# Kernel optimization log

Measured on AMD Instinct MI355X. Metric: run time of the kernel, lower is better.

The kernel has to match this reference:

```python
import jax, jax.numpy as jnp
import numpy as np

B, L, V, H = 2, 2048, 1024, 16
HD = V // H  # head size 64
EPS = 1e-3   # keras LayerNormalization default


def setup_inputs() -> dict:
    key = jax.random.key(0)
    ks = jax.random.split(key, 10)
    scale = 1.0 / np.sqrt(V)
    return {
        "query": jax.random.normal(ks[0], (B, L, V), jnp.float32),
        "key_t": jax.random.normal(ks[1], (B, L, V), jnp.float32),
        "value": jax.random.normal(ks[2], (B, L, V), jnp.float32),
        "Wq": jax.random.normal(ks[3], (H, V, HD), jnp.float32) * scale,
        "Wk": jax.random.normal(ks[4], (H, V, HD), jnp.float32) * scale,
        "Wv": jax.random.normal(ks[5], (H, V, HD), jnp.float32) * scale,
        "gamma": jnp.ones((V,), jnp.float32),
        "beta": jnp.zeros((V,), jnp.float32),
        "query_mask": jax.random.randint(ks[6], (B, L), 0, 2, jnp.int32),
        "value_mask": jax.random.randint(ks[7], (B, L), 0, 2, jnp.int32),
    }


def reference(query, key_t, value, Wq, Wk, Wv, gamma, beta, query_mask, value_mask):
    qm = query_mask.astype(jnp.float32)  # (B,L)
    vm = value_mask.astype(jnp.float32)  # (B,L)

    # per-head no-bias Dense projections, batched over heads
    Q = jnp.einsum('blv,hvd->bhld', query, Wq)
    K = jnp.einsum('blv,hvd->bhld', key_t, Wk)
    Vh = jnp.einsum('blv,hvd->bhld', value, Wv)

    scores = jnp.einsum('bhld,bhmd->bhlm', Q, K) / jnp.sqrt(jnp.float32(HD))
    attn = jax.nn.softmax(scores, axis=-1)

    # post-softmax multiplicative masking (faithful to original)
    tri = jnp.tril(jnp.ones((L, L), jnp.float32))  # (L,L) causal
    attn = attn * tri[None, None, :, :]
    attn = attn * qm[:, None, :, None] * vm[:, None, None, :]

    heads = jnp.einsum('bhlm,bhmd->bhld', attn, Vh)
    x = heads.transpose(0, 2, 1, 3).reshape(B, L, V)  # concat heads

    # dropout is identity at inference
    y = x + query
    mu = jnp.mean(y, axis=-1, keepdims=True)
    var = jnp.mean((y - mu) ** 2, axis=-1, keepdims=True)
    return gamma * (y - mu) * jax.lax.rsqrt(var + EPS) + beta
```

## Files before the change

### kernel.cpp

```cpp
#include <hip/hip_runtime.h>
#include <math.h>

constexpr int NB = 2;
constexpr int SL = 2048;
constexpr int NV = 1024;
constexpr int NH = 16;
constexpr int DH = 64;
constexpr int NT = SL / 64;
constexpr float LN_EPS = 1e-3f;

typedef __bf16 bf16_t;
typedef __bf16 v8bf __attribute__((ext_vector_type(8)));
typedef float  v4f  __attribute__((ext_vector_type(4)));

__device__ __forceinline__ v8bf cvt8(float4 a, float4 b) {
  v8bf v;
  v[0] = (bf16_t)a.x; v[1] = (bf16_t)a.y; v[2] = (bf16_t)a.z; v[3] = (bf16_t)a.w;
  v[4] = (bf16_t)b.x; v[5] = (bf16_t)b.y; v[6] = (bf16_t)b.z; v[7] = (bf16_t)b.w;
  return v;
}
__device__ __forceinline__ unsigned pack_bf16(float a, float b) {
  unsigned short ua = __builtin_bit_cast(unsigned short, (bf16_t)a);
  unsigned short ub = __builtin_bit_cast(unsigned short, (bf16_t)b);
  return (unsigned)ua | ((unsigned)ub << 16);
}
__device__ __forceinline__ void async_cp16(const void* g, void* l) {
  __builtin_amdgcn_global_load_lds(
      (const __attribute__((address_space(1))) unsigned int*)g,
      (__attribute__((address_space(3))) unsigned int*)l, 16, 0, 0);
}

__global__ __launch_bounds__(256)
void wcvt(const float* __restrict__ Wq, const float* __restrict__ Wk,
          const float* __restrict__ Wv, bf16_t* __restrict__ Wt) {
  __shared__ float ls[64][65];
  const int z = blockIdx.z;
  const float* W = z == 0 ? Wq : (z == 1 ? Wk : Wv);
  const float sc = z == 0 ? 0.125f * 1.44269504f : 1.0f;
  const int h = blockIdx.y, v0 = blockIdx.x * 64;
  const int t = threadIdx.x;
  const int rr = t >> 4, c4 = t & 15;
  const float* src = W + ((size_t)h * NV + v0) * DH;
#pragma unroll
  for (int it = 0; it < 4; ++it) {
    float4 f = *(const float4*)(src + (size_t)(rr + it * 16) * DH + c4 * 4);
    ls[rr + it * 16][c4 * 4 + 0] = f.x;
    ls[rr + it * 16][c4 * 4 + 1] = f.y;
    ls[rr + it * 16][c4 * 4 + 2] = f.z;
    ls[rr + it * 16][c4 * 4 + 3] = f.w;
  }
  __syncthreads();
  const int dd = t >> 2, vq = t & 3;
  bf16_t tmp[16];
#pragma unroll
  for (int i = 0; i < 16; ++i) tmp[i] = (bf16_t)(ls[vq * 16 + i][dd] * sc);
  bf16_t* dst = Wt + ((size_t)z * NV + h * 64 + dd) * NV + v0 + vq * 16;
  *(v8bf*)dst = *(v8bf*)&tmp[0];
  *(v8bf*)(dst + 8) = *(v8bf*)&tmp[8];
}

__global__ __launch_bounds__(256, 3)
void proj_mfma(const float* __restrict__ A0, const float* __restrict__ A1,
               const float* __restrict__ A2, const bf16_t* __restrict__ Wtb,
               const int* __restrict__ vmask,
               bf16_t* __restrict__ O0, bf16_t* __restrict__ O1,
               bf16_t* __restrict__ O2) {
  __shared__ __align__(16) float  As[2][128 * 32];
  __shared__ __align__(16) bf16_t Wsh[2][128 * 32];

  const int z = blockIdx.z;
  const float*  A   = z == 0 ? A0 : (z == 1 ? A1 : A2);
  bf16_t*       out = z == 0 ? O0 : (z == 1 ? O1 : O2);
  const bf16_t* W   = Wtb + (size_t)z * NV * NV;

  const int t = threadIdx.x, w = t >> 6, lane = t & 63;
  const int g = lane >> 4, lx = lane & 15;
  const int m0 = blockIdx.x * 128, n0 = blockIdx.y * 128;
  const int rbase = (w >> 1) * 64, cbase = (w & 1) * 64;

  auto stageA = [&](int k0, int buf) {
#pragma unroll
    for (int s = 0; s < 4; ++s) {
      const int r = w * 32 + s * 8 + (lane >> 3);
      const int c = (lane & 7) ^ (r & 7);
      async_cp16(A + (size_t)(m0 + r) * NV + k0 + c * 4,
                 (char*)As[buf] + (w * 32 + s * 8) * 128);
    }
  };
  auto stageW = [&](int k0, int buf) {
#pragma unroll
    for (int s = 0; s < 2; ++s) {
      const int r = w * 32 + s * 16 + (lane >> 2);
      const int c = (lane & 3) ^ (r & 3);
      async_cp16(W + (size_t)(n0 + r) * NV + k0 + c * 8,
                 (char*)Wsh[buf] + (w * 32 + s * 16) * 64);
    }
  };

  v4f acc[4][4] = {};
  stageA(0, 0);
  stageW(0, 0);

  for (int k0 = 0; k0 < NV; k0 += 32) {
    const int buf = (k0 >> 5) & 1;
    __syncthreads();
    if (k0 + 32 < NV) { stageA(k0 + 32, buf ^ 1); stageW(k0 + 32, buf ^ 1); }
    v8bf af[4], wf[4];
#pragma unroll
    for (int rt = 0; rt < 4; ++rt) {
      const int row = rbase + rt * 16 + lx;
      const int sw = row & 7;
      float4 f0 = *(const float4*)((const char*)As[buf] + row * 128 + ((2 * g)     ^ sw) * 16);
      float4 f1 = *(const float4*)((const char*)As[buf] + row * 128 + ((2 * g + 1) ^ sw) * 16);
      af[rt] = cvt8(f0, f1);
    }
#pragma unroll
    for (int ct = 0; ct < 4; ++ct) {
      const int row = cbase + ct * 16 + lx;
      wf[ct] = *(const v8bf*)((const char*)Wsh[buf] + row * 64 + (g ^ (row & 3)) * 16);
    }
#pragma unroll
    for (int rt = 0; rt < 4; ++rt)
#pragma unroll
      for (int ct = 0; ct < 4; ++ct)
        acc[rt][ct] = __builtin_amdgcn_mfma_f32_16x16x32_bf16(
            af[rt], wf[ct], acc[rt][ct], 0, 0, 0);
  }

  if (z < 2) {
#pragma unroll
    for (int rt = 0; rt < 4; ++rt) {
#pragma unroll
      for (int reg = 0; reg < 4; ++reg) {
        const int row = m0 + rbase + rt * 16 + g * 4 + reg;
        const int b = row >> 11, l = row & (SL - 1);
#pragma unroll
        for (int ct = 0; ct < 4; ++ct) {
          const int n = n0 + cbase + ct * 16 + lx;
          const int h = n >> 6, d = n & 63;
          out[((size_t)(b * NH + h) * SL + l) * DH + d] = (bf16_t)acc[rt][ct][reg];
        }
      }
    }
  } else {
#pragma unroll
    for (int rt = 0; rt < 4; ++rt) {
      const int row = m0 + rbase + rt * 16 + g * 4;
      const int b = row >> 11, l = row & (SL - 1);
      float vm0 = (float)vmask[b * SL + l + 0];
      float vm1 = (float)vmask[b * SL + l + 1];
      float vm2 = (float)vmask[b * SL + l + 2];
      float vm3 = (float)vmask[b * SL + l + 3];
#pragma unroll
      for (int ct = 0; ct < 4; ++ct) {
        const int n = n0 + cbase + ct * 16 + lx;
        const int h = n >> 6, d = n & 63;
        uint2 u = {pack_bf16(acc[rt][ct][0] * vm0, acc[rt][ct][1] * vm1),
                   pack_bf16(acc[rt][ct][2] * vm2, acc[rt][ct][3] * vm3)};
        *(uint2*)&out[((size_t)(b * NH + h) * DH + d) * SL + l] = u;
      }
    }
  }
}

__global__ __launch_bounds__(256, 3)
void attn_mfma(const bf16_t* __restrict__ Qg, const bf16_t* __restrict__ Kg,
               const bf16_t* __restrict__ Vtg_all, const int* __restrict__ qmask,
               float* __restrict__ Xout) {
  struct LoopBufs { bf16_t kbuf[2][64 * 64]; bf16_t vbuf[2][64 * 64]; };
  union __align__(16) SU { LoopBufs lp; float Obuf[2][64][36]; };
  __shared__ SU su;
  __shared__ bf16_t Ps[64][72];
  __shared__ float sums[2][64];

  const int id = blockIdx.x;
  const int bh = (id & 7) | ((id >> 8) << 3);
  const int qb = 31 - ((id >> 3) & 31);
  const int t = threadIdx.x, w = t >> 6, lane = t & 63;
  const int g = lane >> 4, lx = lane & 15;
  const int mh = w >> 1, qh = w & 1;
  const int b = bh >> 4, h = bh & 15;
  const int l0 = qb * 64;

  const bf16_t* Kb  = Kg + (size_t)bh * SL * DH;
  const bf16_t* Vtg = Vtg_all + (size_t)bh * DH * SL;

  v8bf qf[2][2];
#pragma unroll
  for (int qt = 0; qt < 2; ++qt)
#pragma unroll
    for (int ks = 0; ks < 2; ++ks)
      qf[qt][ks] = *(const v8bf*)&Qg[((size_t)bh * SL + l0 + qh * 32 + qt * 16 + lx) * DH +
                                     ks * 32 + g * 8];

  v4f O[2][4] = {};
  float suml[2] = {0.f, 0.f};

  auto stageK = [&](int mb, int buf) {
#pragma unroll
    for (int s = 0; s < 2; ++s) {
      const int r = w * 16 + s * 8 + (lane >> 3);
      const int c = (lane & 7) ^ (r & 7);
      async_cp16(Kb + (size_t)(mb + r) * DH + c * 8,
                 (char*)su.lp.kbuf[buf] + (w * 16 + s * 8) * 128);
    }
  };
  auto stageV = [&](int mb, int buf) {
#pragma unroll
    for (int s = 0; s < 2; ++s) {
      const int r = w * 16 + s * 8 + (lane >> 3);
      const int c = (lane & 7) ^ (r & 7);
      async_cp16(Vtg + (size_t)r * SL + mb + c * 8,
                 (char*)su.lp.vbuf[buf] + (w * 16 + s * 8) * 128);
    }
  };

  stageK(0, 0);
  stageV(0, 0);

  for (int mt = 0; mt <= qb; ++mt) {
    const int m0 = mt * 64, pb = mt & 1;
    __syncthreads();
    if (mt + 1 < NT)  stageK(m0 + 64, pb ^ 1);
    if (mt + 1 <= qb) stageV(m0 + 64, pb ^ 1);

    v4f S[2][2] = {};
#pragma unroll
    for (int ks = 0; ks < 2; ++ks)
#pragma unroll
      for (int mt2 = 0; mt2 < 2; ++mt2) {
        const int row = mh * 32 + mt2 * 16 + lx;
        const int slot = (ks * 4 + g) ^ (row & 7);
        v8bf kf = *(const v8bf*)((const char*)su.lp.kbuf[pb] + row * 128 + slot * 16);
#pragma unroll
        for (int qt = 0; qt < 2; ++qt)
          S[mt2][qt] = __builtin_amdgcn_mfma_f32_16x16x32_bf16(
              kf, qf[qt][ks], S[mt2][qt], 0, 0, 0);
      }

    const bool diag = (mt == qb);
#pragma unroll
    for (int mt2 = 0; mt2 < 2; ++mt2)
#pragma unroll
      for (int qt = 0; qt < 2; ++qt) {
        float e0 = __builtin_amdgcn_exp2f(S[mt2][qt][0]);
        float e1 = __builtin_amdgcn_exp2f(S[mt2][qt][1]);
        float e2 = __builtin_amdgcn_exp2f(S[mt2][qt][2]);
        float e3 = __builtin_amdgcn_exp2f(S[mt2][qt][3]);
        suml[qt] += (e0 + e1) + (e2 + e3);
        if (diag) {
          const int ml = mh * 32 + mt2 * 16 + g * 4;
          const int ql = qh * 32 + qt * 16 + lx;
          e0 = (ml + 0 <= ql) ? e0 : 0.f;
          e1 = (ml + 1 <= ql) ? e1 : 0.f;
          e2 = (ml + 2 <= ql) ? e2 : 0.f;
          e3 = (ml + 3 <= ql) ? e3 : 0.f;
        }
        uint2 u = {pack_bf16(e0, e1), pack_bf16(e2, e3)};
        *(uint2*)&Ps[qh * 32 + qt * 16 + lx][mh * 32 + mt2 * 16 + g * 4] = u;
      }

    v8bf pf[2];
#pragma unroll
    for (int qt = 0; qt < 2; ++qt)
      pf[qt] = *(const v8bf*)&Ps[qh * 32 + qt * 16 + lx][mh * 32 + g * 8];
#pragma unroll
    for (int dt = 0; dt < 4; ++dt) {
      const int row = dt * 16 + lx;
      const int slot = (mh * 4 + g) ^ (row & 7);
      v8bf vf = *(const v8bf*)((const char*)su.lp.vbuf[pb] + row * 128 + slot * 16);
#pragma unroll
      for (int qt = 0; qt < 2; ++qt)
        O[qt][dt] = __builtin_amdgcn_mfma_f32_16x16x32_bf16(
            pf[qt], vf, O[qt][dt], 0, 0, 0);
    }
  }

  for (int mt = qb + 1; mt < NT; ++mt) {
    const int pb = mt & 1;
    __syncthreads();
    if (mt + 1 < NT) stageK(mt * 64 + 64, pb ^ 1);
    v4f S[2][2] = {};
#pragma unroll
    for (int ks = 0; ks < 2; ++ks)
#pragma unroll
      for (int mt2 = 0; mt2 < 2; ++mt2) {
        const int row = mh * 32 + mt2 * 16 + lx;
        const int slot = (ks * 4 + g) ^ (row & 7);
        v8bf kf = *(const v8bf*)((const char*)su.lp.kbuf[pb] + row * 128 + slot * 16);
#pragma unroll
        for (int qt = 0; qt < 2; ++qt)
          S[mt2][qt] = __builtin_amdgcn_mfma_f32_16x16x32_bf16(
              kf, qf[qt][ks], S[mt2][qt], 0, 0, 0);
      }
#pragma unroll
    for (int mt2 = 0; mt2 < 2; ++mt2)
#pragma unroll
      for (int qt = 0; qt < 2; ++qt)
        suml[qt] += (__builtin_amdgcn_exp2f(S[mt2][qt][0]) +
                     __builtin_amdgcn_exp2f(S[mt2][qt][1])) +
                    (__builtin_amdgcn_exp2f(S[mt2][qt][2]) +
                     __builtin_amdgcn_exp2f(S[mt2][qt][3]));
  }

  suml[0] += __shfl_xor(suml[0], 16); suml[0] += __shfl_xor(suml[0], 32);
  suml[1] += __shfl_xor(suml[1], 16); suml[1] += __shfl_xor(suml[1], 32);
  __syncthreads();
  if (g == 0) {
    sums[mh][qh * 32 + lx]      = suml[0];
    sums[mh][qh * 32 + 16 + lx] = suml[1];
  }
  if (mh == 0) {
#pragma unroll
    for (int qt = 0; qt < 2; ++qt)
#pragma unroll
      for (int dt = 0; dt < 4; ++dt)
        *(v4f*)&su.Obuf[qh][dt * 16 + lx][qt * 16 + g * 4] = O[qt][dt];
  }
  __syncthreads();
  if (mh == 1) {
#pragma unroll
    for (int qt = 0; qt < 2; ++qt) {
#pragma unroll
      for (int dt = 0; dt < 4; ++dt)
        O[qt][dt] += *(const v4f*)&su.Obuf[qh][dt * 16 + lx][qt * 16 + g * 4];
#pragma unroll
      for (int reg = 0; reg < 4; ++reg) {
        const int ql = qh * 32 + qt * 16 + g * 4 + reg;
        const int q = l0 + ql;
        const float den = sums[0][ql] + sums[1][ql];
        const float inv = (float)qmask[b * SL + q] / den;
#pragma unroll
        for (int dt = 0; dt < 4; ++dt)
          Xout[((size_t)(b * SL + q)) * NV + h * DH + dt * 16 + lx] =
              O[qt][dt][reg] * inv;
      }
    }
  }
}

__global__ __launch_bounds__(256)
void ln_kernel(const float* __restrict__ X, const float* __restrict__ query,
               const float* __restrict__ gamma, const float* __restrict__ beta,
               float* __restrict__ out) {
  const int row0 = blockIdx.x * 2;
  const int t = threadIdx.x;
  float4 gv = *(const float4*)(gamma + t * 4);
  float4 bv = *(const float4*)(beta + t * 4);
  float y[2][4];
  float s[2], ss[2];
#pragma unroll
  for (int r = 0; r < 2; ++r) {
    float4 xv = *(const float4*)(X + (size_t)(row0 + r) * NV + t * 4);
    float4 qv = *(const float4*)(query + (size_t)(row0 + r) * NV + t * 4);
    y[r][0] = xv.x + qv.x; y[r][1] = xv.y + qv.y;
    y[r][2] = xv.z + qv.z; y[r][3] = xv.w + qv.w;
    s[r]  = (y[r][0] + y[r][1]) + (y[r][2] + y[r][3]);
    ss[r] = (y[r][0]*y[r][0] + y[r][1]*y[r][1]) + (y[r][2]*y[r][2] + y[r][3]*y[r][3]);
  }
#pragma unroll
  for (int off = 1; off < 64; off <<= 1) {
    s[0]  += __shfl_xor(s[0], off);  ss[0] += __shfl_xor(ss[0], off);
    s[1]  += __shfl_xor(s[1], off);  ss[1] += __shfl_xor(ss[1], off);
  }
  __shared__ float wsum[2][2][4];
  const int wid = t >> 6;
  if ((t & 63) == 0) {
    wsum[0][0][wid] = s[0]; wsum[0][1][wid] = ss[0];
    wsum[1][0][wid] = s[1]; wsum[1][1][wid] = ss[1];
  }
  __syncthreads();
#pragma unroll
  for (int r = 0; r < 2; ++r) {
    float sr  = (wsum[r][0][0] + wsum[r][0][1]) + (wsum[r][0][2] + wsum[r][0][3]);
    float ssr = (wsum[r][1][0] + wsum[r][1][1]) + (wsum[r][1][2] + wsum[r][1][3]);
    const float mu   = sr * (1.f / NV);
    const float var  = ssr * (1.f / NV) - mu * mu;
    const float rstd = rsqrtf(var + LN_EPS);
    float4 o;
    o.x = gv.x * (y[r][0] - mu) * rstd + bv.x;
    o.y = gv.y * (y[r][1] - mu) * rstd + bv.y;
    o.z = gv.z * (y[r][2] - mu) * rstd + bv.z;
    o.w = gv.w * (y[r][3] - mu) * rstd + bv.w;
    *(float4*)(out + (size_t)(row0 + r) * NV + t * 4) = o;
  }
}

extern "C" void kernel_launch(void* const* d_in, const int* in_sizes, int n_in,
                              void* d_out, int out_size, void* d_ws, size_t ws_size,
                              hipStream_t stream) {
  const float* query = (const float*)d_in[0];
  const float* key_t = (const float*)d_in[1];
  const float* value = (const float*)d_in[2];
  const float* Wq    = (const float*)d_in[3];
  const float* Wk    = (const float*)d_in[4];
  const float* Wv    = (const float*)d_in[5];
  const float* gamma = (const float*)d_in[6];
  const float* beta  = (const float*)d_in[7];
  const int*   qmask = (const int*)d_in[8];
  const int*   vmask = (const int*)d_in[9];
  float* out = (float*)d_out;

  const size_t per = (size_t)NB * NH * SL * DH;
  bf16_t* Qws = (bf16_t*)d_ws;
  bf16_t* Kws = Qws + per;
  bf16_t* Vws = Kws + per;
  bf16_t* Wtb = Vws + per;

  wcvt<<<dim3(16, 16, 3), 256, 0, stream>>>(Wq, Wk, Wv, Wtb);
  proj_mfma<<<dim3(32, 8, 3), 256, 0, stream>>>(query, key_t, value, Wtb,
                                                vmask, Qws, Kws, Vws);
  attn_mfma<<<1024, 256, 0, stream>>>(Qws, Kws, Vws, qmask, out);
  ln_kernel<<<NB * SL / 2, 256, 0, stream>>>(out, query, gamma, beta, out);
}
```

Before: 226.8 us.

## Convert A to bf16 in projection staging; drop LDS staging in attention

The projection kernel now loads fp32 activations into registers, converts them to bf16 once and writes them to swizzled LDS with a 64-wide K step, instead of async-copying fp32 and converting at every fragment read. This lowers the launch-bounds occupancy target to 2. The attention kernel drops the LDS double buffering of K and V and reads fragments straight from global memory in 128-key tiles, keeping only the P tile in LDS and applying the causal mask on every active tile. This removes barriers and LDS traffic but depends on cache hits for the global fragment loads, and the new P write/read path has no visible barrier between waves.

```diff
diff --git a/kernel.cpp b/kernel.cpp
--- a/kernel.cpp
+++ b/kernel.cpp
@@ -6,19 +6,12 @@
 constexpr int NV = 1024;
 constexpr int NH = 16;
 constexpr int DH = 64;
-constexpr int NT = SL / 64;
 constexpr float LN_EPS = 1e-3f;
 
 typedef __bf16 bf16_t;
 typedef __bf16 v8bf __attribute__((ext_vector_type(8)));
 typedef float  v4f  __attribute__((ext_vector_type(4)));
 
-__device__ __forceinline__ v8bf cvt8(float4 a, float4 b) {
-  v8bf v;
-  v[0] = (bf16_t)a.x; v[1] = (bf16_t)a.y; v[2] = (bf16_t)a.z; v[3] = (bf16_t)a.w;
-  v[4] = (bf16_t)b.x; v[5] = (bf16_t)b.y; v[6] = (bf16_t)b.z; v[7] = (bf16_t)b.w;
-  return v;
-}
 __device__ __forceinline__ unsigned pack_bf16(float a, float b) {
   unsigned short ua = __builtin_bit_cast(unsigned short, (bf16_t)a);
   unsigned short ub = __builtin_bit_cast(unsigned short, (bf16_t)b);
@@ -59,14 +52,14 @@
   *(v8bf*)(dst + 8) = *(v8bf*)&tmp[8];
 }
 
-__global__ __launch_bounds__(256, 3)
+__global__ __launch_bounds__(256, 2)
 void proj_mfma(const float* __restrict__ A0, const float* __restrict__ A1,
                const float* __restrict__ A2, const bf16_t* __restrict__ Wtb,
                const int* __restrict__ vmask,
                bf16_t* __restrict__ O0, bf16_t* __restrict__ O1,
                bf16_t* __restrict__ O2) {
-  __shared__ __align__(16) float  As[2][128 * 32];
-  __shared__ __align__(16) bf16_t Wsh[2][128 * 32];
+  __shared__ __align__(16) bf16_t Asb[2][128 * 64];
+  __shared__ __align__(16) bf16_t Wsb[2][128 * 64];
 
   const int z = blockIdx.z;
   const float*  A   = z == 0 ? A0 : (z == 1 ? A1 : A2);
@@ -78,53 +71,66 @@
   const int m0 = blockIdx.x * 128, n0 = blockIdx.y * 128;
   const int rbase = (w >> 1) * 64, cbase = (w & 1) * 64;
 
-  auto stageA = [&](int k0, int buf) {
+  const int ar_off = lane >> 4, ac = lane & 15;
+  float4 ar[8];
+  auto gloadA = [&](int k0) {
+#pragma unroll
+    for (int s = 0; s < 8; ++s)
+      ar[s] = *(const float4*)(A + (size_t)(m0 + w * 32 + s * 4 + ar_off) * NV +
+                               k0 + ac * 4);
+  };
+  auto writeA = [&](int buf) {
+#pragma unroll
+    for (int s = 0; s < 8; ++s) {
+      const int r = w * 32 + s * 4 + ar_off;
+      uint2 u = {pack_bf16(ar[s].x, ar[s].y), pack_bf16(ar[s].z, ar[s].w)};
+      *(uint2*)((char*)Asb[buf] + r * 128 + (((ac >> 1) ^ (r & 7)) * 16) +
+                (ac & 1) * 8) = u;
+    }
+  };
+  auto stageW = [&](int k0, int buf) {
 #pragma unroll
     for (int s = 0; s < 4; ++s) {
       const int r = w * 32 + s * 8 + (lane >> 3);
       const int c = (lane & 7) ^ (r & 7);
-      async_cp16(A + (size_t)(m0 + r) * NV + k0 + c * 4,
-                 (char*)As[buf] + (w * 32 + s * 8) * 128);
+      async_cp16(W + (size_t)(n0 + r) * NV + k0 + c * 8,
+                 (char*)Wsb[buf] + (w * 32 + s * 8) * 128);
     }
   };
-  auto stageW = [&](int k0, int buf) {
-#pragma unroll
-    for (int s = 0; s < 2; ++s) {
-      const int r = w * 32 + s * 16 + (lane >> 2);
-      const int c = (lane & 3) ^ (r & 3);
-      async_cp16(W + (size_t)(n0 + r) * NV + k0 + c * 8,
-                 (char*)Wsh[buf] + (w * 32 + s * 16) * 64);
-    }
-  };
 
   v4f acc[4][4] = {};
-  stageA(0, 0);
+
+  gloadA(0);
   stageW(0, 0);
-
-  for (int k0 = 0; k0 < NV; k0 += 32) {
-    const int buf = (k0 >> 5) & 1;
-    __syncthreads();
-    if (k0 + 32 < NV) { stageA(k0 + 32, buf ^ 1); stageW(k0 + 32, buf ^ 1); }
-    v8bf af[4], wf[4];
-#pragma unroll
-    for (int rt = 0; rt < 4; ++rt) {
-      const int row = rbase + rt * 16 + lx;
-      const int sw = row & 7;
-      float4 f0 = *(const float4*)((const char*)As[buf] + row * 128 + ((2 * g)     ^ sw) * 16);
-      float4 f1 = *(const float4*)((const char*)As[buf] + row * 128 + ((2 * g + 1) ^ sw) * 16);
-      af[rt] = cvt8(f0, f1);
-    }
-#pragma unroll
-    for (int ct = 0; ct < 4; ++ct) {
-      const int row = cbase + ct * 16 + lx;
-      wf[ct] = *(const v8bf*)((const char*)Wsh[buf] + row * 64 + (g ^ (row & 3)) * 16);
-    }
-#pragma unroll
-    for (int rt = 0; rt < 4; ++rt)
-#pragma unroll
-      for (int ct = 0; ct < 4; ++ct)
-        acc[rt][ct] = __builtin_amdgcn_mfma_f32_16x16x32_bf16(
-            af[rt], wf[ct], acc[rt][ct], 0, 0, 0);
+  writeA(0);
+  __syncthreads();
+
+  for (int it = 0; it < 16; ++it) {
+    const int buf = it & 1;
+    if (it < 15) { gloadA((it + 1) * 64); stageW((it + 1) * 64, buf ^ 1); }
+#pragma unroll
+    for (int ks = 0; ks < 2; ++ks) {
+      v8bf af[4], wf[4];
+#pragma unroll
+      for (int rt = 0; rt < 4; ++rt) {
+        const int row = rbase + rt * 16 + lx;
+        af[rt] = *(const v8bf*)((const char*)Asb[buf] + row * 128 +
+                                (((ks * 4 + g) ^ (row & 7)) * 16));
+      }
+#pragma unroll
+      for (int ct = 0; ct < 4; ++ct) {
+        const int row = cbase + ct * 16 + lx;
+        wf[ct] = *(const v8bf*)((const char*)Wsb[buf] + row * 128 +
+                                (((ks * 4 + g) ^ (row & 7)) * 16));
+      }
+#pragma unroll
+      for (int rt = 0; rt < 4; ++rt)
+#pragma unroll
+        for (int ct = 0; ct < 4; ++ct)
+          acc[rt][ct] = __builtin_amdgcn_mfma_f32_16x16x32_bf16(
+              af[rt], wf[ct], acc[rt][ct], 0, 0, 0);
+    }
+    if (it < 15) { writeA(buf ^ 1); __syncthreads(); }
   }
 
   if (z < 2) {
@@ -167,11 +173,11 @@
 void attn_mfma(const bf16_t* __restrict__ Qg, const bf16_t* __restrict__ Kg,
                const bf16_t* __restrict__ Vtg_all, const int* __restrict__ qmask,
                float* __restrict__ Xout) {
-  struct LoopBufs { bf16_t kbuf[2][64 * 64]; bf16_t vbuf[2][64 * 64]; };
-  union __align__(16) SU { LoopBufs lp; float Obuf[2][64][36]; };
+  union __align__(16) SU {
+    bf16_t Ps[64][136];
+    struct { float Obuf[2][64][36]; float sums[2][64]; } ep;
+  };
   __shared__ SU su;
-  __shared__ bf16_t Ps[64][72];
-  __shared__ float sums[2][64];
 
   const int id = blockIdx.x;
   const int bh = (id & 7) | ((id >> 8) << 3);
@@ -181,6 +187,7 @@
   const int mh = w >> 1, qh = w & 1;
   const int b = bh >> 4, h = bh & 15;
   const int l0 = qb * 64;
+  const int nact = qb / 2 + 1;
 
   const bf16_t* Kb  = Kg + (size_t)bh * SL * DH;
   const bf16_t* Vtg = Vtg_all + (size_t)bh * DH * SL;
@@ -196,51 +203,26 @@
   v4f O[2][4] = {};
   float suml[2] = {0.f, 0.f};
 
-  auto stageK = [&](int mb, int buf) {
-#pragma unroll
-    for (int s = 0; s < 2; ++s) {
-      const int r = w * 16 + s * 8 + (lane >> 3);
-      const int c = (lane & 7) ^ (r & 7);
-      async_cp16(Kb + (size_t)(mb + r) * DH + c * 8,
-                 (char*)su.lp.kbuf[buf] + (w * 16 + s * 8) * 128);
-    }
-  };
-  auto stageV = [&](int mb, int buf) {
-#pragma unroll
-    for (int s = 0; s < 2; ++s) {
-      const int r = w * 16 + s * 8 + (lane >> 3);
-      const int c = (lane & 7) ^ (r & 7);
-      async_cp16(Vtg + (size_t)r * SL + mb + c * 8,
-                 (char*)su.lp.vbuf[buf] + (w * 16 + s * 8) * 128);
-    }
-  };
-
-  stageK(0, 0);
-  stageV(0, 0);
-
-  for (int mt = 0; mt <= qb; ++mt) {
-    const int m0 = mt * 64, pb = mt & 1;
-    __syncthreads();
-    if (mt + 1 < NT)  stageK(m0 + 64, pb ^ 1);
-    if (mt + 1 <= qb) stageV(m0 + 64, pb ^ 1);
-
-    v4f S[2][2] = {};
-#pragma unroll
-    for (int ks = 0; ks < 2; ++ks)
-#pragma unroll
-      for (int mt2 = 0; mt2 < 2; ++mt2) {
-        const int row = mh * 32 + mt2 * 16 + lx;
-        const int slot = (ks * 4 + g) ^ (row & 7);
-        v8bf kf = *(const v8bf*)((const char*)su.lp.kbuf[pb] + row * 128 + slot * 16);
+  for (int mt = 0; mt < nact; ++mt) {
+    const int m0 = mt * 128;
+    v4f S[4][2];
+#pragma unroll
+    for (int mt2 = 0; mt2 < 4; ++mt2) {
+      S[mt2][0] = (v4f){0.f, 0.f, 0.f, 0.f};
+      S[mt2][1] = (v4f){0.f, 0.f, 0.f, 0.f};
+#pragma unroll
+      for (int ks = 0; ks < 2; ++ks) {
+        v8bf kf = *(const v8bf*)&Kb[(size_t)(m0 + mh * 64 + mt2 * 16 + lx) * DH +
+                                    ks * 32 + g * 8];
 #pragma unroll
         for (int qt = 0; qt < 2; ++qt)
           S[mt2][qt] = __builtin_amdgcn_mfma_f32_16x16x32_bf16(
               kf, qf[qt][ks], S[mt2][qt], 0, 0, 0);
       }
-
-    const bool diag = (mt == qb);
-#pragma unroll
-    for (int mt2 = 0; mt2 < 2; ++mt2)
+    }
+
+#pragma unroll
+    for (int mt2 = 0; mt2 < 4; ++mt2)
 #pragma unroll
       for (int qt = 0; qt < 2; ++qt) {
         float e0 = __builtin_amdgcn_exp2f(S[mt2][qt][0]);
@@ -248,74 +230,72 @@
         float e2 = __builtin_amdgcn_exp2f(S[mt2][qt][2]);
         float e3 = __builtin_amdgcn_exp2f(S[mt2][qt][3]);
         suml[qt] += (e0 + e1) + (e2 + e3);
-        if (diag) {
-          const int ml = mh * 32 + mt2 * 16 + g * 4;
-          const int ql = qh * 32 + qt * 16 + lx;
-          e0 = (ml + 0 <= ql) ? e0 : 0.f;
-          e1 = (ml + 1 <= ql) ? e1 : 0.f;
-          e2 = (ml + 2 <= ql) ? e2 : 0.f;
-          e3 = (ml + 3 <= ql) ? e3 : 0.f;
-        }
+        const int ml = m0 + mh * 64 + mt2 * 16 + g * 4;
+        const int ql = l0 + qh * 32 + qt * 16 + lx;
+        e0 = (ml + 0 <= ql) ? e0 : 0.f;
+        e1 = (ml + 1 <= ql) ? e1 : 0.f;
+        e2 = (ml + 2 <= ql) ? e2 : 0.f;
+        e3 = (ml + 3 <= ql) ? e3 : 0.f;
         uint2 u = {pack_bf16(e0, e1), pack_bf16(e2, e3)};
-        *(uint2*)&Ps[qh * 32 + qt * 16 + lx][mh * 32 + mt2 * 16 + g * 4] = u;
-      }
-
-    v8bf pf[2];
-#pragma unroll
-    for (int qt = 0; qt < 2; ++qt)
-      pf[qt] = *(const v8bf*)&Ps[qh * 32 + qt * 16 + lx][mh * 32 + g * 8];
-#pragma unroll
-    for (int dt = 0; dt < 4; ++dt) {
-      const int row = dt * 16 + lx;
-      const int slot = (mh * 4 + g) ^ (row & 7);
-      v8bf vf = *(const v8bf*)((const char*)su.lp.vbuf[pb] + row * 128 + slot * 16);
+        *(uint2*)&su.Ps[qh * 32 + qt * 16 + lx][mh * 64 + mt2 * 16 + g * 4] = u;
+      }
+
+#pragma unroll
+    for (int ks = 0; ks < 2; ++ks) {
+      v8bf pf[2];
 #pragma unroll
       for (int qt = 0; qt < 2; ++qt)
-        O[qt][dt] = __builtin_amdgcn_mfma_f32_16x16x32_bf16(
-            pf[qt], vf, O[qt][dt], 0, 0, 0);
-    }
-  }
-
-  for (int mt = qb + 1; mt < NT; ++mt) {
-    const int pb = mt & 1;
-    __syncthreads();
-    if (mt + 1 < NT) stageK(mt * 64 + 64, pb ^ 1);
-    v4f S[2][2] = {};
-#pragma unroll
-    for (int ks = 0; ks < 2; ++ks)
-#pragma unroll
-      for (int mt2 = 0; mt2 < 2; ++mt2) {
-        const int row = mh * 32 + mt2 * 16 + lx;
-        const int slot = (ks * 4 + g) ^ (row & 7);
-        v8bf kf = *(const v8bf*)((const char*)su.lp.kbuf[pb] + row * 128 + slot * 16);
+        pf[qt] = *(const v8bf*)&su.Ps[qh * 32 + qt * 16 + lx][mh * 64 + ks * 32 + g * 8];
+#pragma unroll
+      for (int dt = 0; dt < 4; ++dt) {
+        v8bf vf = *(const v8bf*)&Vtg[(size_t)(dt * 16 + lx) * SL + m0 + mh * 64 +
+                                     ks * 32 + g * 8];
 #pragma unroll
         for (int qt = 0; qt < 2; ++qt)
-          S[mt2][qt] = __builtin_amdgcn_mfma_f32_16x16x32_bf16(
-              kf, qf[qt][ks], S[mt2][qt], 0, 0, 0);
-      }
-#pragma unroll
-    for (int mt2 = 0; mt2 < 2; ++mt2)
+          O[qt][dt] = __builtin_amdgcn_mfma_f32_16x16x32_bf16(
+              pf[qt], vf, O[qt][dt], 0, 0, 0);
+      }
+    }
+  }
+
+  for (int mt = nact; mt < SL / 128; ++mt) {
+    const int m0 = mt * 128;
+#pragma unroll
+    for (int mt2 = 0; mt2 < 4; ++mt2) {
+      v4f S2[2];
+      S2[0] = (v4f){0.f, 0.f, 0.f, 0.f};
+      S2[1] = (v4f){0.f, 0.f, 0.f, 0.f};
+#pragma unroll
+      for (int ks = 0; ks < 2; ++ks) {
+        v8bf kf = *(const v8bf*)&Kb[(size_t)(m0 + mh * 64 + mt2 * 16 + lx) * DH +
+                                    ks * 32 + g * 8];
+#pragma unroll
+        for (int qt = 0; qt < 2; ++qt)
+          S2[qt] = __builtin_amdgcn_mfma_f32_16x16x32_bf16(
+              kf, qf[qt][ks], S2[qt], 0, 0, 0);
+      }
 #pragma unroll
       for (int qt = 0; qt < 2; ++qt)
-        suml[qt] += (__builtin_amdgcn_exp2f(S[mt2][qt][0]) +
-                     __builtin_amdgcn_exp2f(S[mt2][qt][1])) +
-                    (__builtin_amdgcn_exp2f(S[mt2][qt][2]) +
-                     __builtin_amdgcn_exp2f(S[mt2][qt][3]));
+        suml[qt] += (__builtin_amdgcn_exp2f(S2[qt][0]) +
+                     __builtin_amdgcn_exp2f(S2[qt][1])) +
+                    (__builtin_amdgcn_exp2f(S2[qt][2]) +
+                     __builtin_amdgcn_exp2f(S2[qt][3]));
+    }
   }
 
   suml[0] += __shfl_xor(suml[0], 16); suml[0] += __shfl_xor(suml[0], 32);
   suml[1] += __shfl_xor(suml[1], 16); suml[1] += __shfl_xor(suml[1], 32);
   __syncthreads();
   if (g == 0) {
-    sums[mh][qh * 32 + lx]      = suml[0];
-    sums[mh][qh * 32 + 16 + lx] = suml[1];
+    su.ep.sums[mh][qh * 32 + lx]      = suml[0];
+    su.ep.sums[mh][qh * 32 + 16 + lx] = suml[1];
   }
   if (mh == 0) {
 #pragma unroll
     for (int qt = 0; qt < 2; ++qt)
 #pragma unroll
       for (int dt = 0; dt < 4; ++dt)
-        *(v4f*)&su.Obuf[qh][dt * 16 + lx][qt * 16 + g * 4] = O[qt][dt];
+        *(v4f*)&su.ep.Obuf[qh][dt * 16 + lx][qt * 16 + g * 4] = O[qt][dt];
   }
   __syncthreads();
   if (mh == 1) {
@@ -323,12 +303,12 @@
     for (int qt = 0; qt < 2; ++qt) {
 #pragma unroll
       for (int dt = 0; dt < 4; ++dt)
-        O[qt][dt] += *(const v4f*)&su.Obuf[qh][dt * 16 + lx][qt * 16 + g * 4];
+        O[qt][dt] += *(const v4f*)&su.ep.Obuf[qh][dt * 16 + lx][qt * 16 + g * 4];
 #pragma unroll
       for (int reg = 0; reg < 4; ++reg) {
         const int ql = qh * 32 + qt * 16 + g * 4 + reg;
         const int q = l0 + ql;
-        const float den = sums[0][ql] + sums[1][ql];
+        const float den = su.ep.sums[0][ql] + su.ep.sums[1][ql];
         const float inv = (float)qmask[b * SL + q] / den;
 #pragma unroll
         for (int dt = 0; dt < 4; ++dt)
```

Result: slower. 306.2 us (+35.0%).
